# Performance work log

Measured on AMD Instinct MI355X. Metric: run time of the kernel, lower is better.

The kernel has to match this reference:

```python
import jax, jax.numpy as jnp
import numpy as np

B, S, D = 1, 2048, 1024
F = 1408            # expert intermediate dim
E = 16              # num experts
K = 2               # top_k
CAP_FACTOR = 1.25


def _mlp(h, wg, wu, wd):
    # DeepSeek-style gated MLP (SwiGLU, no bias)
    return (jax.nn.silu(h @ wg) * (h @ wu)) @ wd


def setup_inputs() -> dict:
    key = jax.random.key(0)
    ks = jax.random.split(key, 10)
    sd = 0.02
    return {
        "x": jax.random.normal(ks[0], (B, S, D), jnp.float32),
        "router_w": jax.random.normal(ks[1], (D, E), jnp.float32) * sd,
        "router_b": jnp.zeros((E,), jnp.float32),
        "w_gate": jax.random.normal(ks[2], (E, D, F), jnp.float32) * sd,
        "w_up": jax.random.normal(ks[3], (E, D, F), jnp.float32) * sd,
        "w_down": jax.random.normal(ks[4], (E, F, D), jnp.float32) * sd,
        "sw_gate": jax.random.normal(ks[5], (D, F), jnp.float32) * sd,
        "sw_up": jax.random.normal(ks[6], (D, F), jnp.float32) * sd,
        "sw_down": jax.random.normal(ks[7], (F, D), jnp.float32) * sd,
    }


def reference(x, router_w, router_b, w_gate, w_up, w_down, sw_gate, sw_up, sw_down):
    b, s, d = x.shape
    N = b * s
    NK = N * K
    C = int(np.ceil(CAP_FACTOR * NK / E))  # per-expert capacity

    x_tokens = x.reshape(N, d)

    # Router: softmax -> top-k -> renormalize
    logits = x_tokens @ router_w + router_b           # [N, E]
    probs = jax.nn.softmax(logits, axis=-1)
    vals, idx = jax.lax.top_k(probs, K)               # [N, K]
    vals = vals / (jnp.sum(vals, axis=-1, keepdims=True) + 1e-9)
    idx_flat = idx.reshape(NK)                        # int expert ids
    vals_flat = vals.reshape(NK)

    # Position within each expert's buffer = rank in flattened (token, k) order.
    # Same math as (cumsum(one_hot)*one_hot).sum(-1)-1 in the original.
    oh_e = jax.nn.one_hot(idx_flat, E, dtype=x.dtype)             # [NK, E] (small)
    pos = (jnp.cumsum(oh_e, axis=0) * oh_e).sum(axis=1) - 1       # [NK]
    within = (pos < C).astype(x.dtype)                            # capacity mask
    pos_c = jnp.clip(pos, 0, C - 1).astype(jnp.int32)

    # Dispatch: scatter tokens into per-expert buffers. Positions are unique
    # per expert, so scatter-add equals the dense one-hot einsum exactly.
    token_ids = jnp.arange(NK) // K
    x_pair = x_tokens[token_ids] * within[:, None]                # [NK, D]
    expert_inputs = jnp.zeros((E, C, d), x.dtype).at[idx_flat, pos_c].add(x_pair)

    # Grouped expert MLPs
    expert_outputs = jax.vmap(_mlp)(expert_inputs, w_gate, w_up, w_down)  # [E, C, D]

    # Combine: gather back and weight by renormalized router probs
    gathered = expert_outputs[idx_flat, pos_c] * (vals_flat * within)[:, None]
    output_tokens = gathered.reshape(N, K, d).sum(axis=1)         # [N, D]

    return x + _mlp(x, sw_gate, sw_up, sw_down) + output_tokens.reshape(b, s, d)
```

## Files before the change

### kernel.cpp

```cpp
#include <hip/hip_runtime.h>
#include <hip/hip_bf16.h>

#define TOKENS 2048
#define DIM    1024
#define FDIM   1408
#define NEXP   16
#define NK     (TOKENS * 2)
#define CAP    320
#define RPAD   384

typedef __attribute__((ext_vector_type(4))) float f32x4;
typedef __attribute__((ext_vector_type(8))) short s16x8;
typedef __attribute__((ext_vector_type(4))) short s16x4;

__device__ __forceinline__ short f2bf(float f) {
    unsigned int u = __float_as_uint(f);
    u += 0x7FFFu + ((u >> 16) & 1u);
    return (short)(u >> 16);
}
__device__ __forceinline__ float bf2f(short s) {
    return __uint_as_float(((unsigned int)(unsigned short)s) << 16);
}

#define GLDS16(gp, lp) __builtin_amdgcn_global_load_lds(                     \
    (const __attribute__((address_space(1))) unsigned int*)(gp),             \
    (__attribute__((address_space(3))) unsigned int*)(lp), 16, 0, 0)

struct GSeg {
    const short* A; long aStride; int aRpad;
    const short* B0; const short* B1; long bStride;
    short* Out; long oStride; int oRpad;
    const int* cnt; int Mb, Nb, N, K, nblocks;
};
struct WSeg { const float* in; short* out; int K, N, mats, nblocks; };

__device__ void wchunk_dev(const WSeg& W, int bid)
{
    const int spm = W.K >> 3;
    const int mat = bid / spm, s = bid % spm;
    const float* in  = W.in  + (size_t)mat * W.K * W.N + (size_t)s * 8 * W.N;
    short* out = W.out + (size_t)mat * W.K * W.N + (size_t)s * W.N * 8;
    const int t = threadIdx.x;
    const int iters = (W.N + 511) >> 9;
    for (int it = 0; it < iters; it++) {
        const int n = it * 512 + 2 * t;
        if (n >= W.N) break;
        const float* src = in + n;
        s16x8 o0, o1;
#pragma unroll
        for (int j = 0; j < 8; j++) {
            float2 v = *(const float2*)(src + (size_t)j * W.N);
            o0[j] = f2bf(v.x);
            o1[j] = f2bf(v.y);
        }
        *(s16x8*)(out + (size_t)n * 8)     = o0;
        *(s16x8*)(out + (size_t)n * 8 + 8) = o1;
    }
}

__global__ __launch_bounds__(256) void router_kernel(
    const float* __restrict__ x, const float* __restrict__ rw,
    const float* __restrict__ rb, int* __restrict__ idx_flat,
    float* __restrict__ vals_flat)
{
    __shared__ float lg[16][17];
    const int t  = threadIdx.x;
    const int tl = t >> 4;
    const int e  = t & 15;
    const int token = blockIdx.x * 16 + tl;
    const float* xr = x + (size_t)token * DIM;

    float acc = 0.f;
    for (int d4 = 0; d4 < DIM / 4; d4++) {
        float4 xv = *(const float4*)(xr + d4 * 4);
        acc += xv.x * rw[(d4 * 4 + 0) * NEXP + e];
        acc += xv.y * rw[(d4 * 4 + 1) * NEXP + e];
        acc += xv.z * rw[(d4 * 4 + 2) * NEXP + e];
        acc += xv.w * rw[(d4 * 4 + 3) * NEXP + e];
    }
    lg[tl][e] = acc + rb[e];
    __syncthreads();

    if (t < 16) {
        float l[16];
#pragma unroll
        for (int j = 0; j < 16; j++) l[j] = lg[t][j];
        float m = l[0];
#pragma unroll
        for (int j = 1; j < 16; j++) m = fmaxf(m, l[j]);
        float p[16], den = 0.f;
#pragma unroll
        for (int j = 0; j < 16; j++) { p[j] = __expf(l[j] - m); den += p[j]; }
        int i1 = -1; float b1 = -1e30f;
#pragma unroll
        for (int j = 0; j < 16; j++) if (p[j] > b1) { b1 = p[j]; i1 = j; }
        int i2 = -1; float b2 = -1e30f;
#pragma unroll
        for (int j = 0; j < 16; j++) if (j != i1 && p[j] > b2) { b2 = p[j]; i2 = j; }
        float v1 = b1 / den, v2 = b2 / den;
        float s = v1 + v2 + 1e-9f;
        int tok = blockIdx.x * 16 + t;
        idx_flat[tok * 2 + 0] = i1;
        idx_flat[tok * 2 + 1] = i2;
        vals_flat[tok * 2 + 0] = v1 / s;
        vals_flat[tok * 2 + 1] = v2 / s;
    }
}

__global__ void scan_kernel(const int* __restrict__ idx_flat,
                            const float* __restrict__ vals,
                            int* __restrict__ dst, float* __restrict__ wgt,
                            int* __restrict__ cnt)
{
    const int lane = threadIdx.x;
    int base[16];
#pragma unroll
    for (int e = 0; e < 16; e++) base[e] = 0;

    for (int c = 0; c < NK / 64; c++) {
        int i = c * 64 + lane;
        int e = idx_flat[i];
        unsigned long long m[16];
#pragma unroll
        for (int ee = 0; ee < 16; ee++) m[ee] = __ballot(e == ee);
        unsigned long long mym = 0ULL; int myb = 0;
#pragma unroll
        for (int ee = 0; ee < 16; ee++) {
            bool sel = (e == ee);
            mym = sel ? m[ee] : mym;
            myb = sel ? base[ee] : myb;
        }
        int pos = myb + (int)__popcll(mym & ((1ULL << lane) - 1ULL));
        bool within = pos < CAP;
        dst[i] = within ? (e * RPAD + pos) : -1;
        wgt[i] = within ? vals[i] : 0.f;
#pragma unroll
        for (int ee = 0; ee < 16; ee++) base[ee] += (int)__popcll(m[ee]);
    }
    if (lane < 16) cnt[lane] = base[lane] < CAP ? base[lane] : CAP;
}

__device__ void xconv_dev(const float* __restrict__ x, short* __restrict__ xb, int bid)
{
    const int token = bid * 2 + (threadIdx.x >> 7);
    const int c = threadIdx.x & 127;
    const float* src = x + (size_t)token * DIM + c * 8;
    float4 v0 = *(const float4*)(src);
    float4 v1 = *(const float4*)(src + 4);
    s16x8 o;
    o[0] = f2bf(v0.x); o[1] = f2bf(v0.y); o[2] = f2bf(v0.z); o[3] = f2bf(v0.w);
    o[4] = f2bf(v1.x); o[5] = f2bf(v1.y); o[6] = f2bf(v1.z); o[7] = f2bf(v1.w);
    *(s16x8*)(xb + (size_t)c * (TOKENS * 8) + (size_t)token * 8) = o;
}

__device__ void scatter_dev(const float* __restrict__ x, const int* __restrict__ dst,
                            const int* __restrict__ idx_flat, short* __restrict__ ex,
                            int bid)
{
    const int i = bid * 2 + (threadIdx.x >> 7);
    const int d0 = dst[i];
    if (d0 < 0) return;
    const int e = idx_flat[i];
    const int pos = d0 - e * RPAD;
    const int token = i >> 1;
    const int c = threadIdx.x & 127;
    const float* src = x + (size_t)token * DIM + c * 8;
    float4 v0 = *(const float4*)(src);
    float4 v1 = *(const float4*)(src + 4);
    s16x8 o;
    o[0] = f2bf(v0.x); o[1] = f2bf(v0.y); o[2] = f2bf(v0.z); o[3] = f2bf(v0.w);
    o[4] = f2bf(v1.x); o[5] = f2bf(v1.y); o[6] = f2bf(v1.z); o[7] = f2bf(v1.w);
    *(s16x8*)(ex + (size_t)e * (DIM * RPAD) + (size_t)c * (RPAD * 8) +
              (size_t)pos * 8) = o;
}

__global__ __launch_bounds__(256) void mid_kernel(
    WSeg w0, WSeg w1, WSeg w2, WSeg w3,
    const float* __restrict__ x, short* __restrict__ xb,
    const int* __restrict__ dst, const int* __restrict__ idx_flat,
    short* __restrict__ ex)
{
    int bid = blockIdx.x;
    if (bid < w0.nblocks) { wchunk_dev(w0, bid); return; }
    bid -= w0.nblocks;
    if (bid < w1.nblocks) { wchunk_dev(w1, bid); return; }
    bid -= w1.nblocks;
    if (bid < w2.nblocks) { wchunk_dev(w2, bid); return; }
    bid -= w2.nblocks;
    if (bid < w3.nblocks) { wchunk_dev(w3, bid); return; }
    bid -= w3.nblocks;
    if (bid < TOKENS / 2) { xconv_dev(x, xb, bid); return; }
    bid -= TOKENS / 2;
    scatter_dev(x, dst, idx_flat, ex, bid);
}

template <int NMAT>
__device__ void gemm_dev(const GSeg& S, int bid)
{
    constexpr int BUFS = 4096 * (1 + NMAT);
    __shared__ short lds[2 * BUFS];

    const int cpx = S.nblocks >> 3;
    const int lid = (bid & 7) * cpx + (bid >> 3);
    const int mb  = lid % S.Mb;
    const int t1  = lid / S.Mb;
    const int nb  = t1 % S.Nb;
    const int g   = t1 / S.Nb;
    const int m0 = mb * 128, n0 = nb * 128;
    if (S.cnt != nullptr && m0 >= S.cnt[g]) return;

    const int tid = threadIdx.x, lane = tid & 63, w = tid >> 6;
    const int wr = w >> 1, wc = w & 1, ln = lane & 15, kg = lane >> 4;

    const int N = S.N, K = S.K;
    const short* Ag  = S.A  + (size_t)g * S.aStride + (size_t)m0 * 8;
    const short* Bg0 = S.B0 + (size_t)g * S.bStride + (size_t)n0 * 8;
    const short* Bg1 = nullptr;
    if constexpr (NMAT == 2) Bg1 = S.B1 + (size_t)g * S.bStride + (size_t)n0 * 8;

    const size_t aR8 = (size_t)S.aRpad * 8;
    const size_t n8  = (size_t)N * 8;

    const int srow = tid & 127, sslab = tid >> 7;
    const short* aS0 = Ag  + sslab * aR8 + srow * 8;
    const short* aS1 = Ag  + (2 + sslab) * aR8 + srow * 8;
    const short* bS00 = Bg0 + sslab * n8 + srow * 8;
    const short* bS01 = Bg0 + (2 + sslab) * n8 + srow * 8;
    const short* bS10 = nullptr, *bS11 = nullptr;
    if constexpr (NMAT == 2) {
        bS10 = Bg1 + sslab * n8 + srow * 8;
        bS11 = Bg1 + (2 + sslab) * n8 + srow * 8;
    }

    const int dA0 = w * 512, dA1 = 2048 + w * 512;

    auto STG = [&](int buf, int ks) {
        const size_t ka = (size_t)ks * 4 * aR8;
        const size_t kb = (size_t)ks * 4 * n8;
        short* base = lds + buf * BUFS;
        GLDS16(aS0 + ka,  base + dA0);
        GLDS16(aS1 + ka,  base + dA1);
        GLDS16(bS00 + kb, base + 4096 + dA0);
        GLDS16(bS01 + kb, base + 4096 + dA1);
        if constexpr (NMAT == 2) {
            GLDS16(bS10 + kb, base + 8192 + dA0);
            GLDS16(bS11 + kb, base + 8192 + dA1);
        }
    };

    const int aO = kg * 1024 + (wr * 64 + ln) * 8;
    const int bO = kg * 1024 + (wc * 64 + ln) * 8;

    f32x4 acc[NMAT][4][4] = {};

    const int nt = K / 32;
    STG(0, 0); STG(1, 1);
    int cur = 0;
    for (int ks = 0; ks < nt; ks++) {
        if (ks + 1 < nt) {
            if constexpr (NMAT == 2) asm volatile("s_waitcnt vmcnt(6)" ::: "memory");
            else                     asm volatile("s_waitcnt vmcnt(4)" ::: "memory");
        } else {
            asm volatile("s_waitcnt vmcnt(0)" ::: "memory");
        }
        __builtin_amdgcn_s_barrier();
        __builtin_amdgcn_sched_barrier(0);

        const short* base = lds + cur * BUFS;
        s16x8 af[4];
#pragma unroll
        for (int m = 0; m < 4; m++)
            af[m] = *(const s16x8*)(base + aO + m * 128);
        s16x8 bf[NMAT][4];
#pragma unroll
        for (int mat = 0; mat < NMAT; mat++)
#pragma unroll
            for (int nf = 0; nf < 4; nf++)
                bf[mat][nf] = *(const s16x8*)(base + 4096 + mat * 4096 + bO + nf * 128);

        __builtin_amdgcn_s_setprio(1);
#pragma unroll
        for (int nf = 0; nf < 4; nf++)
#pragma unroll
            for (int m = 0; m < 4; m++)
#pragma unroll
                for (int mat = 0; mat < NMAT; mat++)
                    acc[mat][m][nf] = __builtin_amdgcn_mfma_f32_16x16x32_bf16(
                        af[m], bf[mat][nf], acc[mat][m][nf], 0, 0, 0);
        __builtin_amdgcn_s_setprio(0);
        __builtin_amdgcn_sched_barrier(0);
        __builtin_amdgcn_s_barrier();

        if (ks + 2 < nt) STG(cur, ks + 2);
        cur ^= 1;
    }

#pragma unroll
    for (int m = 0; m < 4; m++) {
#pragma unroll
        for (int nf = 0; nf < 4; nf++) {
            const int row = m0 + wr * 64 + m * 16 + kg * 4;
            const int col = n0 + wc * 64 + nf * 16 + ln;
#pragma unroll
            for (int j = 0; j < 4; j++) {
                if constexpr (NMAT == 2) {
                    float gv = acc[0][m][nf][j];
                    float uv = acc[1][m][nf][j];
                    float v = gv / (1.f + __expf(-gv)) * uv;
                    S.Out[(size_t)g * S.oStride + (size_t)(col >> 3) * (S.oRpad * 8) +
                          (size_t)(row + j) * 8 + (col & 7)] = f2bf(v);
                } else {
                    S.Out[(size_t)g * S.oStride + (size_t)(row + j) * N + col] =
                        f2bf(acc[0][m][nf][j]);
                }
            }
        }
    }
}

__global__ __launch_bounds__(256, 2) void gateup_kernel(GSeg s0, GSeg s1,
                                                        WSeg w0, WSeg w1)
{
    int bid = blockIdx.x;
    if (bid < s0.nblocks) { gemm_dev<2>(s0, bid); return; }
    bid -= s0.nblocks;
    if (bid < s1.nblocks) { gemm_dev<2>(s1, bid); return; }
    bid -= s1.nblocks;
    if (bid < w0.nblocks) { wchunk_dev(w0, bid); return; }
    bid -= w0.nblocks;
    wchunk_dev(w1, bid);
}

__global__ __launch_bounds__(256, 2) void down_kernel(GSeg s0, GSeg s1)
{
    int bid = blockIdx.x;
    if (bid < s0.nblocks) { gemm_dev<1>(s0, bid); return; }
    bid -= s0.nblocks;
    gemm_dev<1>(s1, bid);
}

__global__ __launch_bounds__(256) void combine_kernel(
    const float* __restrict__ x, const short* __restrict__ shout,
    const short* __restrict__ eout, const int* __restrict__ dst,
    const float* __restrict__ wgt, float* __restrict__ out)
{
    const int t = blockIdx.x;
    const int d = threadIdx.x * 4;
    size_t o = (size_t)t * DIM + d;
    float4 xv = *(const float4*)(x + o);
    s16x4 sv = *(const s16x4*)(shout + o);
    float r0 = xv.x + bf2f(sv[0]);
    float r1 = xv.y + bf2f(sv[1]);
    float r2 = xv.z + bf2f(sv[2]);
    float r3 = xv.w + bf2f(sv[3]);
#pragma unroll
    for (int k = 0; k < 2; k++) {
        int di = dst[t * 2 + k];
        if (di >= 0) {
            float wv = wgt[t * 2 + k];
            s16x4 ev = *(const s16x4*)(eout + (size_t)di * DIM + d);
            r0 += wv * bf2f(ev[0]);
            r1 += wv * bf2f(ev[1]);
            r2 += wv * bf2f(ev[2]);
            r3 += wv * bf2f(ev[3]);
        }
    }
    float4 rv = {r0, r1, r2, r3};
    *(float4*)(out + o) = rv;
}

extern "C" void kernel_launch(void* const* d_in, const int* in_sizes, int n_in,
                              void* d_out, int out_size, void* d_ws, size_t ws_size,
                              hipStream_t stream)
{
    const float* x   = (const float*)d_in[0];
    const float* rw  = (const float*)d_in[1];
    const float* rb  = (const float*)d_in[2];
    const float* wg  = (const float*)d_in[3];
    const float* wu  = (const float*)d_in[4];
    const float* wd  = (const float*)d_in[5];
    const float* swg = (const float*)d_in[6];
    const float* swu = (const float*)d_in[7];
    const float* swd = (const float*)d_in[8];
    float* out = (float*)d_out;

    char* wp = (char*)d_ws;
    auto alloc = [&](size_t b) { char* p = wp; wp += (b + 255) & ~(size_t)255; return p; };
    int*   idx_flat = (int*)alloc((size_t)NK * 4);
    float* vals     = (float*)alloc((size_t)NK * 4);
    int*   dst      = (int*)alloc((size_t)NK * 4);
    float* wgt      = (float*)alloc((size_t)NK * 4);
    int*   cnt      = (int*)alloc(64);
    short* xb       = (short*)alloc((size_t)TOKENS * DIM * 2);
    short* ex       = (short*)alloc((size_t)NEXP * RPAD * DIM * 2);
    short* acte     = (short*)alloc((size_t)NEXP * RPAD * FDIM * 2);
    short* acts     = (short*)alloc((size_t)TOKENS * FDIM * 2);
    short* eout     = (short*)alloc((size_t)NEXP * RPAD * DIM * 2);
    short* shout    = (short*)alloc((size_t)TOKENS * DIM * 2);
    short* wgC      = (short*)alloc((size_t)NEXP * DIM * FDIM * 2);
    short* wuC      = (short*)alloc((size_t)NEXP * DIM * FDIM * 2);
    short* wdC      = (short*)alloc((size_t)NEXP * DIM * FDIM * 2);
    short* swgC     = (short*)alloc((size_t)DIM * FDIM * 2);
    short* swuC     = (short*)alloc((size_t)DIM * FDIM * 2);
    short* swdC     = (short*)alloc((size_t)DIM * FDIM * 2);

    WSeg Wg  = {wg,  wgC,  DIM,  FDIM, NEXP, NEXP * (DIM / 8)};
    WSeg Wu  = {wu,  wuC,  DIM,  FDIM, NEXP, NEXP * (DIM / 8)};
    WSeg Wsg = {swg, swgC, DIM,  FDIM, 1,    DIM / 8};
    WSeg Wsu = {swu, swuC, DIM,  FDIM, 1,    DIM / 8};
    WSeg Wd  = {wd,  wdC,  FDIM, DIM,  NEXP, NEXP * (FDIM / 8)};
    WSeg Wsd = {swd, swdC, FDIM, DIM,  1,    FDIM / 8};

    router_kernel<<<TOKENS / 16, 256, 0, stream>>>(x, rw, rb, idx_flat, vals);
    scan_kernel<<<1, 64, 0, stream>>>(idx_flat, vals, dst, wgt, cnt);

    const int mid_blocks = Wg.nblocks + Wu.nblocks + Wsg.nblocks + Wsu.nblocks
                         + TOKENS / 2 + NK / 2;
    mid_kernel<<<mid_blocks, 256, 0, stream>>>(Wg, Wu, Wsg, Wsu,
                                               x, xb, dst, idx_flat, ex);

    GSeg segGE = {ex, (long)RPAD * DIM, RPAD, wgC, wuC, (long)DIM * FDIM,
                  acte, (long)RPAD * FDIM, RPAD, cnt, 3, 11, FDIM, DIM, 3 * 11 * NEXP};
    GSeg segGS = {xb, 0L, TOKENS, swgC, swuC, 0L,
                  acts, 0L, TOKENS, nullptr, 16, 11, FDIM, DIM, 16 * 11};
    gateup_kernel<<<segGE.nblocks + segGS.nblocks + Wd.nblocks + Wsd.nblocks,
                    256, 0, stream>>>(segGE, segGS, Wd, Wsd);

    GSeg segDE = {acte, (long)RPAD * FDIM, RPAD, wdC, nullptr, (long)DIM * FDIM,
                  eout, (long)RPAD * DIM, 0, cnt, 3, 8, DIM, FDIM, 3 * 8 * NEXP};
    GSeg segDS = {acts, 0L, TOKENS, swdC, nullptr, 0L,
                  shout, 0L, 0, nullptr, 16, 8, DIM, FDIM, 16 * 8};
    down_kernel<<<segDE.nblocks + segDS.nblocks, 256, 0, stream>>>(segDE, segDS);

    combine_kernel<<<TOKENS, 256, 0, stream>>>(x, shout, eout, dst, wgt, out);
}
```

Baseline: 249.5 us.

## Fuse fp32-to-bf16 weight conversion into GEMM B-tile staging

Removes the separate weight conversion passes that wrote bf16 copies of all expert and shared weights. The GEMM now loads fp32 weight tiles into registers, converts them to bf16, and writes them to LDS, pipelined against the MFMA loop. This avoids writing and rereading the converted weights. In exchange, each M block reads fp32 weights, which is twice the bytes of bf16, and it adds VALU conversion and register pressure inside the GEMM loop.

```diff
diff --git a/kernel.cpp b/kernel.cpp
--- a/kernel.cpp
+++ b/kernel.cpp
@@ -28,35 +28,10 @@
 
 struct GSeg {
     const short* A; long aStride; int aRpad;
-    const short* B0; const short* B1; long bStride;
+    const float* B0; const float* B1; long bStride;
     short* Out; long oStride; int oRpad;
     const int* cnt; int Mb, Nb, N, K, nblocks;
 };
-struct WSeg { const float* in; short* out; int K, N, mats, nblocks; };
-
-__device__ void wchunk_dev(const WSeg& W, int bid)
-{
-    const int spm = W.K >> 3;
-    const int mat = bid / spm, s = bid % spm;
-    const float* in  = W.in  + (size_t)mat * W.K * W.N + (size_t)s * 8 * W.N;
-    short* out = W.out + (size_t)mat * W.K * W.N + (size_t)s * W.N * 8;
-    const int t = threadIdx.x;
-    const int iters = (W.N + 511) >> 9;
-    for (int it = 0; it < iters; it++) {
-        const int n = it * 512 + 2 * t;
-        if (n >= W.N) break;
-        const float* src = in + n;
-        s16x8 o0, o1;
-#pragma unroll
-        for (int j = 0; j < 8; j++) {
-            float2 v = *(const float2*)(src + (size_t)j * W.N);
-            o0[j] = f2bf(v.x);
-            o1[j] = f2bf(v.y);
-        }
-        *(s16x8*)(out + (size_t)n * 8)     = o0;
-        *(s16x8*)(out + (size_t)n * 8 + 8) = o1;
-    }
-}
 
 __global__ __launch_bounds__(256) void router_kernel(
     const float* __restrict__ x, const float* __restrict__ rw,
@@ -175,23 +150,13 @@
 }
 
 __global__ __launch_bounds__(256) void mid_kernel(
-    WSeg w0, WSeg w1, WSeg w2, WSeg w3,
     const float* __restrict__ x, short* __restrict__ xb,
     const int* __restrict__ dst, const int* __restrict__ idx_flat,
     short* __restrict__ ex)
 {
     int bid = blockIdx.x;
-    if (bid < w0.nblocks) { wchunk_dev(w0, bid); return; }
-    bid -= w0.nblocks;
-    if (bid < w1.nblocks) { wchunk_dev(w1, bid); return; }
-    bid -= w1.nblocks;
-    if (bid < w2.nblocks) { wchunk_dev(w2, bid); return; }
-    bid -= w2.nblocks;
-    if (bid < w3.nblocks) { wchunk_dev(w3, bid); return; }
-    bid -= w3.nblocks;
     if (bid < TOKENS / 2) { xconv_dev(x, xb, bid); return; }
-    bid -= TOKENS / 2;
-    scatter_dev(x, dst, idx_flat, ex, bid);
+    scatter_dev(x, dst, idx_flat, ex, bid - TOKENS / 2);
 }
 
 template <int NMAT>
@@ -211,40 +176,70 @@
 
     const int tid = threadIdx.x, lane = tid & 63, w = tid >> 6;
     const int wr = w >> 1, wc = w & 1, ln = lane & 15, kg = lane >> 4;
-
     const int N = S.N, K = S.K;
+
     const short* Ag  = S.A  + (size_t)g * S.aStride + (size_t)m0 * 8;
-    const short* Bg0 = S.B0 + (size_t)g * S.bStride + (size_t)n0 * 8;
-    const short* Bg1 = nullptr;
-    if constexpr (NMAT == 2) Bg1 = S.B1 + (size_t)g * S.bStride + (size_t)n0 * 8;
+    const float* Bg0 = S.B0 + (size_t)g * S.bStride + n0;
+    const float* Bg1 = nullptr;
+    if constexpr (NMAT == 2) Bg1 = S.B1 + (size_t)g * S.bStride + n0;
 
     const size_t aR8 = (size_t)S.aRpad * 8;
-    const size_t n8  = (size_t)N * 8;
 
     const int srow = tid & 127, sslab = tid >> 7;
-    const short* aS0 = Ag  + sslab * aR8 + srow * 8;
-    const short* aS1 = Ag  + (2 + sslab) * aR8 + srow * 8;
-    const short* bS00 = Bg0 + sslab * n8 + srow * 8;
-    const short* bS01 = Bg0 + (2 + sslab) * n8 + srow * 8;
-    const short* bS10 = nullptr, *bS11 = nullptr;
+    const short* aS0 = Ag + sslab * aR8 + srow * 8;
+    const short* aS1 = Ag + (2 + sslab) * aR8 + srow * 8;
+    const int dA0 = w * 512, dA1 = 2048 + w * 512;
+
+    const float* bSrc;
+    int bW;
     if constexpr (NMAT == 2) {
-        bS10 = Bg1 + sslab * n8 + srow * 8;
-        bS11 = Bg1 + (2 + sslab) * n8 + srow * 8;
-    }
-
-    const int dA0 = w * 512, dA1 = 2048 + w * 512;
-
-    auto STG = [&](int buf, int ks) {
+        const int c4 = tid & 31, gq = (tid >> 5) & 3, mat = tid >> 7;
+        bSrc = (mat ? Bg1 : Bg0) + (size_t)gq * 8 * N + c4 * 4;
+        bW = 4096 + mat * 4096 + gq * 1024 + c4 * 32;
+    } else {
+        const int c2 = tid & 63, gq = tid >> 6;
+        bSrc = Bg0 + (size_t)gq * 8 * N + c2 * 2;
+        bW = 4096 + gq * 1024 + c2 * 16;
+    }
+
+    float4 bq[8];
+    float2 bd[8];
+
+    auto LOADB = [&](int ks) {
+        const float* p = bSrc + (size_t)ks * 32 * N;
+        if constexpr (NMAT == 2) {
+#pragma unroll
+            for (int j = 0; j < 8; j++) bq[j] = *(const float4*)(p + (size_t)j * N);
+        } else {
+#pragma unroll
+            for (int j = 0; j < 8; j++) bd[j] = *(const float2*)(p + (size_t)j * N);
+        }
+    };
+    auto STGA = [&](int buf, int ks) {
         const size_t ka = (size_t)ks * 4 * aR8;
-        const size_t kb = (size_t)ks * 4 * n8;
         short* base = lds + buf * BUFS;
-        GLDS16(aS0 + ka,  base + dA0);
-        GLDS16(aS1 + ka,  base + dA1);
-        GLDS16(bS00 + kb, base + 4096 + dA0);
-        GLDS16(bS01 + kb, base + 4096 + dA1);
+        GLDS16(aS0 + ka, base + dA0);
+        GLDS16(aS1 + ka, base + dA1);
+    };
+    auto WRITEB = [&](int buf) {
+        short* d = lds + buf * BUFS + bW;
         if constexpr (NMAT == 2) {
-            GLDS16(bS10 + kb, base + 8192 + dA0);
-            GLDS16(bS11 + kb, base + 8192 + dA1);
+            s16x8 o0, o1, o2, o3;
+#pragma unroll
+            for (int j = 0; j < 8; j++) {
+                o0[j] = f2bf(bq[j].x); o1[j] = f2bf(bq[j].y);
+                o2[j] = f2bf(bq[j].z); o3[j] = f2bf(bq[j].w);
+            }
+            *(s16x8*)(d)      = o0;
+            *(s16x8*)(d + 8)  = o1;
+            *(s16x8*)(d + 16) = o2;
+            *(s16x8*)(d + 24) = o3;
+        } else {
+            s16x8 o0, o1;
+#pragma unroll
+            for (int j = 0; j < 8; j++) { o0[j] = f2bf(bd[j].x); o1[j] = f2bf(bd[j].y); }
+            *(s16x8*)(d)     = o0;
+            *(s16x8*)(d + 8) = o1;
         }
     };
 
@@ -252,17 +247,25 @@
     const int bO = kg * 1024 + (wc * 64 + ln) * 8;
 
     f32x4 acc[NMAT][4][4] = {};
-
     const int nt = K / 32;
-    STG(0, 0); STG(1, 1);
+
+    LOADB(0);
+    __builtin_amdgcn_sched_barrier(0);
+    STGA(0, 0);
+    __builtin_amdgcn_sched_barrier(0);
+    asm volatile("s_waitcnt vmcnt(2)" ::: "memory");
+    WRITEB(0);
+    asm volatile("s_waitcnt lgkmcnt(0)" ::: "memory");
+    __builtin_amdgcn_sched_barrier(0);
+    LOADB(1);
+    __builtin_amdgcn_sched_barrier(0);
+    STGA(1, 1);
+    __builtin_amdgcn_sched_barrier(0);
+
     int cur = 0;
     for (int ks = 0; ks < nt; ks++) {
-        if (ks + 1 < nt) {
-            if constexpr (NMAT == 2) asm volatile("s_waitcnt vmcnt(6)" ::: "memory");
-            else                     asm volatile("s_waitcnt vmcnt(4)" ::: "memory");
-        } else {
-            asm volatile("s_waitcnt vmcnt(0)" ::: "memory");
-        }
+        if (ks + 1 < nt) asm volatile("s_waitcnt vmcnt(10)" ::: "memory");
+        else             asm volatile("s_waitcnt vmcnt(0)"  ::: "memory");
         __builtin_amdgcn_s_barrier();
         __builtin_amdgcn_sched_barrier(0);
 
@@ -289,9 +292,21 @@
                         af[m], bf[mat][nf], acc[mat][m][nf], 0, 0, 0);
         __builtin_amdgcn_s_setprio(0);
         __builtin_amdgcn_sched_barrier(0);
+
+        if (ks + 1 < nt) {
+            asm volatile("s_waitcnt vmcnt(2)" ::: "memory");
+            WRITEB(cur ^ 1);
+            asm volatile("s_waitcnt lgkmcnt(0)" ::: "memory");
+        }
+        __builtin_amdgcn_sched_barrier(0);
         __builtin_amdgcn_s_barrier();
 
-        if (ks + 2 < nt) STG(cur, ks + 2);
+        if (ks + 2 < nt) {
+            LOADB(ks + 2);
+            __builtin_amdgcn_sched_barrier(0);
+            STGA(cur, ks + 2);
+            __builtin_amdgcn_sched_barrier(0);
+        }
         cur ^= 1;
     }
 
@@ -318,25 +333,18 @@
     }
 }
 
-__global__ __launch_bounds__(256, 2) void gateup_kernel(GSeg s0, GSeg s1,
-                                                        WSeg w0, WSeg w1)
+__global__ __launch_bounds__(256, 2) void gateup_kernel(GSeg s0, GSeg s1)
 {
     int bid = blockIdx.x;
     if (bid < s0.nblocks) { gemm_dev<2>(s0, bid); return; }
-    bid -= s0.nblocks;
-    if (bid < s1.nblocks) { gemm_dev<2>(s1, bid); return; }
-    bid -= s1.nblocks;
-    if (bid < w0.nblocks) { wchunk_dev(w0, bid); return; }
-    bid -= w0.nblocks;
-    wchunk_dev(w1, bid);
+    gemm_dev<2>(s1, bid - s0.nblocks);
 }
 
 __global__ __launch_bounds__(256, 2) void down_kernel(GSeg s0, GSeg s1)
 {
     int bid = blockIdx.x;
     if (bid < s0.nblocks) { gemm_dev<1>(s0, bid); return; }
-    bid -= s0.nblocks;
-    gemm_dev<1>(s1, bid);
+    gemm_dev<1>(s1, bid - s0.nblocks);
 }
 
 __global__ __launch_bounds__(256) void combine_kernel(
@@ -397,38 +405,21 @@
     short* acts     = (short*)alloc((size_t)TOKENS * FDIM * 2);
     short* eout     = (short*)alloc((size_t)NEXP * RPAD * DIM * 2);
     short* shout    = (short*)alloc((size_t)TOKENS * DIM * 2);
-    short* wgC      = (short*)alloc((size_t)NEXP * DIM * FDIM * 2);
-    short* wuC      = (short*)alloc((size_t)NEXP * DIM * FDIM * 2);
-    short* wdC      = (short*)alloc((size_t)NEXP * DIM * FDIM * 2);
-    short* swgC     = (short*)alloc((size_t)DIM * FDIM * 2);
-    short* swuC     = (short*)alloc((size_t)DIM * FDIM * 2);
-    short* swdC     = (short*)alloc((size_t)DIM * FDIM * 2);
-
-    WSeg Wg  = {wg,  wgC,  DIM,  FDIM, NEXP, NEXP * (DIM / 8)};
-    WSeg Wu  = {wu,  wuC,  DIM,  FDIM, NEXP, NEXP * (DIM / 8)};
-    WSeg Wsg = {swg, swgC, DIM,  FDIM, 1,    DIM / 8};
-    WSeg Wsu = {swu, swuC, DIM,  FDIM, 1,    DIM / 8};
-    WSeg Wd  = {wd,  wdC,  FDIM, DIM,  NEXP, NEXP * (FDIM / 8)};
-    WSeg Wsd = {swd, swdC, FDIM, DIM,  1,    FDIM / 8};
 
     router_kernel<<<TOKENS / 16, 256, 0, stream>>>(x, rw, rb, idx_flat, vals);
     scan_kernel<<<1, 64, 0, stream>>>(idx_flat, vals, dst, wgt, cnt);
 
-    const int mid_blocks = Wg.nblocks + Wu.nblocks + Wsg.nblocks + Wsu.nblocks
-                         + TOKENS / 2 + NK / 2;
-    mid_kernel<<<mid_blocks, 256, 0, stream>>>(Wg, Wu, Wsg, Wsu,
-                                               x, xb, dst, idx_flat, ex);
-
-    GSeg segGE = {ex, (long)RPAD * DIM, RPAD, wgC, wuC, (long)DIM * FDIM,
+    mid_kernel<<<TOKENS / 2 + NK / 2, 256, 0, stream>>>(x, xb, dst, idx_flat, ex);
+
+    GSeg segGE = {ex, (long)RPAD * DIM, RPAD, wg, wu, (long)DIM * FDIM,
                   acte, (long)RPAD * FDIM, RPAD, cnt, 3, 11, FDIM, DIM, 3 * 11 * NEXP};
-    GSeg segGS = {xb, 0L, TOKENS, swgC, swuC, 0L,
+    GSeg segGS = {xb, 0L, TOKENS, swg, swu, 0L,
                   acts, 0L, TOKENS, nullptr, 16, 11, FDIM, DIM, 16 * 11};
-    gateup_kernel<<<segGE.nblocks + segGS.nblocks + Wd.nblocks + Wsd.nblocks,
-                    256, 0, stream>>>(segGE, segGS, Wd, Wsd);
-
-    GSeg segDE = {acte, (long)RPAD * FDIM, RPAD, wdC, nullptr, (long)DIM * FDIM,
+    gateup_kernel<<<segGE.nblocks + segGS.nblocks, 256, 0, stream>>>(segGE, segGS);
+
+    GSeg segDE = {acte, (long)RPAD * FDIM, RPAD, wd, nullptr, (long)DIM * FDIM,
                   eout, (long)RPAD * DIM, 0, cnt, 3, 8, DIM, FDIM, 3 * 8 * NEXP};
-    GSeg segDS = {acts, 0L, TOKENS, swdC, nullptr, 0L,
+    GSeg segDS = {acts, 0L, TOKENS, swd, nullptr, 0L,
                   shout, 0L, 0, nullptr, 16, 8, DIM, FDIM, 16 * 8};
     down_kernel<<<segDE.nblocks + segDS.nblocks, 256, 0, stream>>>(segDE, segDS);
 
```

New measurement: 265.4 us. 6.4% more time.
